# Kernel optimization log

Measured on AMD Instinct MI355X. Metric: run time of the kernel, lower is better.

## Reference

```python
import jax, jax.numpy as jnp
import numpy as np

K = 20
DEPTH = 4
EMB = 1024
NEG = 0.2   # LeakyReLU slope
EPS = 1e-5  # BatchNorm eps (inference mode: running_mean=0, running_var=1)


def _bn_lrelu(x, g, b):
    # inference BatchNorm over channel axis 1 with mean=0, var=1, then LeakyReLU(0.2)
    sh = [1] * x.ndim
    sh[1] = -1
    y = x * (g / jnp.sqrt(1.0 + EPS)).reshape(sh) + b.reshape(sh)
    return jnp.where(y >= 0, y, NEG * y)


def _attention_edge(x, Wq, Wk, Wv):
    # x: (G, N, C). Full self-attention, topk neighbor selection, EdgeConv features.
    C = x.shape[-1]
    q = x @ Wq.T
    k = x @ Wk.T
    v = x @ Wv.T
    att = jax.nn.softmax(jnp.einsum('gnc,gmc->gnm', q, k) / jnp.sqrt(jnp.float32(C)), axis=-1)
    out = jnp.einsum('gnm,gmc->gnc', att, v)
    idx = jax.lax.top_k(att, K)[1]                      # (G,N,K) neighbor indices
    xt = x + out                                        # residual: x + x_sa
    feat = jax.vmap(lambda a, i: a[i])(xt, idx)         # (G,N,K,C) gather
    ctr = jnp.broadcast_to(xt[:, :, None, :], feat.shape)
    return jnp.concatenate([feat - ctr, ctr], axis=-1)  # (G,N,K,2C)


def _seq_graph_feature(x, Wq, Wk, Wv):
    # x: (B, F, C, N) -> (B, 2C, F, N, K); vectorizes the per-sample Python loop
    B, F, C, N = x.shape
    xf = x.reshape(B * F, C, N).transpose(0, 2, 1)      # (G,N,C)
    e = _attention_edge(xf, Wq, Wk, Wv)                 # (G,N,K,2C)
    return e.reshape(B, F, N, K, 2 * C).transpose(0, 4, 1, 2, 3)


def setup_inputs() -> dict:
    key = jax.random.key(0)
    ks = jax.random.split(key, 16)
    d = {}
    d['x'] = jax.random.normal(ks[0], (8, 32, 3, 512), jnp.float32)
    d['Wq1'] = jax.random.normal(ks[1], (3, 3), jnp.float32) * 0.5
    d['Wk1'] = jax.random.normal(ks[2], (3, 3), jnp.float32) * 0.5
    d['Wv1'] = jax.random.normal(ks[3], (3, 3), jnp.float32) * 0.5
    d['Wq2'] = jax.random.normal(ks[4], (64, 64), jnp.float32) * 0.1
    d['Wk2'] = jax.random.normal(ks[5], (64, 64), jnp.float32) * 0.1
    d['Wv2'] = jax.random.normal(ks[6], (64, 64), jnp.float32) * 0.1
    d['conv1_w'] = jax.random.normal(ks[7], (64, 6, DEPTH, 3, 3), jnp.float32) * 0.1
    d['conv2_w'] = jax.random.normal(ks[8], (128, 128), jnp.float32) * 0.05
    d['conv5_w'] = jax.random.normal(ks[9], (EMB, 192), jnp.float32) * 0.05
    d['bn1_g'] = jax.random.uniform(ks[10], (64,), jnp.float32, 0.5, 1.5)
    d['bn1_b'] = jax.random.normal(ks[11], (64,), jnp.float32) * 0.1
    d['bn2_g'] = jax.random.uniform(ks[12], (128,), jnp.float32, 0.5, 1.5)
    d['bn2_b'] = jax.random.normal(ks[13], (128,), jnp.float32) * 0.1
    d['bn5_g'] = jax.random.uniform(ks[14], (EMB,), jnp.float32, 0.5, 1.5)
    d['bn5_b'] = jax.random.normal(ks[15], (EMB,), jnp.float32) * 0.1
    return d


def reference(x, Wq1, Wk1, Wv1, Wq2, Wk2, Wv2, conv1_w, conv2_w, conv5_w,
              bn1_g, bn1_b, bn2_g, bn2_b, bn5_g, bn5_b):
    y = _seq_graph_feature(x, Wq1, Wk1, Wv1)                      # (B,6,F,N,K)
    y = jax.lax.conv_general_dilated(
        y, conv1_w, window_strides=(DEPTH, 2, 1), padding='VALID',
        dimension_numbers=('NCDHW', 'OIDHW', 'NCDHW'))            # (B,64,F',N',K-2)
    y = _bn_lrelu(y, bn1_g, bn1_b)
    x1 = y.max(axis=-1)                                           # (B,64,F',N')
    x1p = x1.transpose(0, 2, 1, 3)                                # (B,F',64,N')
    y = _seq_graph_feature(x1p, Wq2, Wk2, Wv2)                    # (B,128,F',N',K)
    y = jnp.einsum('bcfnk,oc->bofnk', y, conv2_w)                 # 1x1x1 conv3d
    y = _bn_lrelu(y, bn2_g, bn2_b)
    x2 = y.max(axis=-1)                                           # (B,128,F',N')
    y = jnp.concatenate([x1, x2], axis=1)                         # (B,192,F',N')
    y = jnp.einsum('bcfn,oc->bofn', y, conv5_w)                   # 1x1 conv2d
    y = _bn_lrelu(y, bn5_g, bn5_b)
    emb = y.max(axis=-1).transpose(0, 2, 1)                       # (B,F',EMB)
    return emb
```

## Files before the change

### kernel.cpp

```cpp
#include <hip/hip_runtime.h>
#include <hip/hip_bf16.h>
#include <math.h>

typedef float f4 __attribute__((ext_vector_type(4)));

#define NEG 0.2f
#define BN_EPS 1e-5f

#define CE(K,A,B) { unsigned long long _x = K[A], _y = K[B]; bool _s = _x < _y; \
                    K[A] = _s ? _y : _x; K[B] = _s ? _x : _y; }

__device__ __forceinline__ float wred_max_f32(float v) {
  int x = __float_as_int(v), y;
#define STEPM(C) y = __builtin_amdgcn_update_dpp(x, x, C, 0xf, 0xf, false); \
  x = __float_as_int(fmaxf(__int_as_float(x), __int_as_float(y)));
  STEPM(0x111) STEPM(0x112) STEPM(0x114) STEPM(0x118) STEPM(0x142) STEPM(0x143)
#undef STEPM
  return __int_as_float(__builtin_amdgcn_readlane(x, 63));
}
__device__ __forceinline__ float wred_sum_f32(float v) {
  int x = __float_as_int(v), y;
#define STEPS(C) y = __builtin_amdgcn_update_dpp(0, x, C, 0xf, 0xf, true); \
  x = __float_as_int(__int_as_float(x) + __int_as_float(y));
  STEPS(0x111) STEPS(0x112) STEPS(0x114) STEPS(0x118) STEPS(0x142) STEPS(0x143)
#undef STEPS
  return __int_as_float(__builtin_amdgcn_readlane(x, 63));
}
__device__ __forceinline__ unsigned wred16_max_u32(unsigned v) {
  int x = (int)v, y;
#define STEPU(C) y = __builtin_amdgcn_update_dpp(x, x, C, 0xf, 0xf, false); \
  x = (int)((unsigned)x > (unsigned)y ? (unsigned)x : (unsigned)y);
  STEPU(0x111) STEPU(0x112) STEPU(0x114) STEPU(0x118)
#undef STEPU
  unsigned a0 = (unsigned)__builtin_amdgcn_readlane(x, 15);
  unsigned a1 = (unsigned)__builtin_amdgcn_readlane(x, 31);
  unsigned a2 = (unsigned)__builtin_amdgcn_readlane(x, 47);
  unsigned a3 = (unsigned)__builtin_amdgcn_readlane(x, 63);
  unsigned m01 = a0 > a1 ? a0 : a1;
  unsigned m23 = a2 > a3 ? a2 : a3;
  return m01 > m23 ? m01 : m23;
}

__device__ __forceinline__ unsigned sel_round8(unsigned (&hi)[8], unsigned (&lo)[8],
                                               bool do_pop) {
  unsigned gv = wred16_max_u32(hi[0]);
  unsigned long long tied = __ballot(hi[0] == gv);
  unsigned gl;
  if (__popcll(tied) == 1) {
    int wl = __ffsll((long long)tied) - 1;
    gl = (unsigned)__builtin_amdgcn_readlane((int)lo[0], wl);
  } else {
    gl = wred16_max_u32((hi[0] == gv) ? lo[0] : 0u);
  }
  if (do_pop) {
    bool win = (hi[0] == gv) && (lo[0] == gl);
    hi[0] = win ? hi[1] : hi[0]; lo[0] = win ? lo[1] : lo[0];
    hi[1] = win ? hi[2] : hi[1]; lo[1] = win ? lo[2] : lo[1];
    hi[2] = win ? hi[3] : hi[2]; lo[2] = win ? lo[3] : lo[2];
    hi[3] = win ? hi[4] : hi[3]; lo[3] = win ? lo[4] : lo[3];
    hi[4] = win ? hi[5] : hi[4]; lo[4] = win ? lo[5] : lo[4];
    hi[5] = win ? hi[6] : hi[5]; lo[5] = win ? lo[6] : lo[5];
    hi[6] = win ? hi[7] : hi[6]; lo[6] = win ? lo[7] : lo[6];
    hi[7] = win ? 0u    : hi[7]; lo[7] = win ? 0u    : lo[7];
  }
  return gl;
}
__device__ __forceinline__ unsigned sel_round4(unsigned (&hi)[4], unsigned (&lo)[4],
                                               bool do_pop) {
  unsigned gv = wred16_max_u32(hi[0]);
  unsigned long long tied = __ballot(hi[0] == gv);
  unsigned gl;
  if (__popcll(tied) == 1) {
    int wl = __ffsll((long long)tied) - 1;
    gl = (unsigned)__builtin_amdgcn_readlane((int)lo[0], wl);
  } else {
    gl = wred16_max_u32((hi[0] == gv) ? lo[0] : 0u);
  }
  if (do_pop) {
    bool win = (hi[0] == gv) && (lo[0] == gl);
    hi[0] = win ? hi[1] : hi[0]; lo[0] = win ? lo[1] : lo[0];
    hi[1] = win ? hi[2] : hi[1]; lo[1] = win ? lo[2] : lo[1];
    hi[2] = win ? hi[3] : hi[2]; lo[2] = win ? lo[3] : lo[2];
    hi[3] = win ? 0u    : hi[3]; lo[3] = win ? 0u    : lo[3];
  }
  return gl;
}

__global__ __launch_bounds__(256) void qkv1_k(const float* __restrict__ x,
    const float* __restrict__ Wk, const float* __restrict__ Wv,
    float* __restrict__ k1, float* __restrict__ v1) {
#pragma clang fp contract(off)
  int g = blockIdx.y;
  int n = blockIdx.x * 256 + threadIdx.x;
  const float* xr = x + (size_t)g * 1536;
  float x0 = xr[n], x1v = xr[512 + n], x2v = xr[1024 + n];
  f4 kd, vd;
#pragma unroll
  for (int o = 0; o < 3; ++o) {
    kd[o] = x0 * Wk[o*3+0] + x1v * Wk[o*3+1] + x2v * Wk[o*3+2];
    vd[o] = x0 * Wv[o*3+0] + x1v * Wv[o*3+1] + x2v * Wv[o*3+2];
  }
  kd[3] = 0.f; vd[3] = 0.f;
  *(f4*)(k1 + ((size_t)g * 512 + n) * 4) = kd;
  *(f4*)(v1 + ((size_t)g * 512 + n) * 4) = vd;
}

__global__ __launch_bounds__(256) void attn1_k(const float* __restrict__ x,
    const float* __restrict__ Wq, const float* __restrict__ k1,
    const float* __restrict__ v1, float* __restrict__ xt1p, int* __restrict__ idx1) {
  __shared__ f4 kl[512];
  __shared__ f4 vl[512];
  int t = threadIdx.x, g = blockIdx.y;
  int w = t >> 6, l = t & 63;
  int nb = blockIdx.x * 16;
  const f4* kgp = (const f4*)(k1 + (size_t)g * 2048);
  const f4* vgp = (const f4*)(v1 + (size_t)g * 2048);
  for (int i = t; i < 512; i += 256) { kl[i] = kgp[i]; vl[i] = vgp[i]; }
  __syncthreads();
  const float* xr = x + (size_t)g * 1536;
  for (int rp = 0; rp < 2; ++rp) {
    int nA = nb + rp * 8 + w;
    int nB = nA + 4;
    float xA0 = xr[nA], xA1 = xr[512 + nA], xA2 = xr[1024 + nA];
    float xB0 = xr[nB], xB1 = xr[512 + nB], xB2 = xr[1024 + nB];
    float qA0, qA1, qA2, qB0, qB1, qB2;
    float aA[8], aB[8];
    {
#pragma clang fp contract(off)
      qA0 = xA0*Wq[0] + xA1*Wq[1] + xA2*Wq[2];
      qA1 = xA0*Wq[3] + xA1*Wq[4] + xA2*Wq[5];
      qA2 = xA0*Wq[6] + xA1*Wq[7] + xA2*Wq[8];
      qB0 = xB0*Wq[0] + xB1*Wq[1] + xB2*Wq[2];
      qB1 = xB0*Wq[3] + xB1*Wq[4] + xB2*Wq[5];
      qB2 = xB0*Wq[6] + xB1*Wq[7] + xB2*Wq[8];
#pragma unroll
      for (int j = 0; j < 8; ++j) {
        f4 kk = kl[l + 64 * j];
        aA[j] = (qA0*kk[0] + qA1*kk[1] + qA2*kk[2]) / sqrtf(3.0f);
        aB[j] = (qB0*kk[0] + qB1*kk[1] + qB2*kk[2]) / sqrtf(3.0f);
      }
    }
    float mxA = aA[0], mxB = aB[0];
#pragma unroll
    for (int j = 1; j < 8; ++j) { mxA = fmaxf(mxA, aA[j]); mxB = fmaxf(mxB, aB[j]); }
    mxA = wred_max_f32(mxA); mxB = wred_max_f32(mxB);
    float wsA = 0.f, wsB = 0.f;
#pragma unroll
    for (int j = 0; j < 8; ++j) {
      aA[j] = expf(aA[j] - mxA); wsA += aA[j];
      aB[j] = expf(aB[j] - mxB); wsB += aB[j];
    }
    wsA = wred_sum_f32(wsA); wsB = wred_sum_f32(wsB);
#pragma unroll
    for (int j = 0; j < 8; ++j) { aA[j] = aA[j] / wsA; aB[j] = aB[j] / wsB; }
    float oA0 = 0.f, oA1 = 0.f, oA2 = 0.f, oB0 = 0.f, oB1 = 0.f, oB2 = 0.f;
#pragma unroll
    for (int j = 0; j < 8; ++j) {
      f4 vv = vl[l + 64 * j];
      oA0 += aA[j] * vv[0]; oA1 += aA[j] * vv[1]; oA2 += aA[j] * vv[2];
      oB0 += aB[j] * vv[0]; oB1 += aB[j] * vv[1]; oB2 += aB[j] * vv[2];
    }
    oA0 = wred_sum_f32(oA0); oA1 = wred_sum_f32(oA1); oA2 = wred_sum_f32(oA2);
    oB0 = wred_sum_f32(oB0); oB1 = wred_sum_f32(oB1); oB2 = wred_sum_f32(oB2);
    if (l == 0) {
      float* xo = xt1p + ((size_t)g * 512 + nA) * 4;
      xo[0] = xA0 + oA0; xo[1] = xA1 + oA1; xo[2] = xA2 + oA2;
      float* xo2 = xt1p + ((size_t)g * 512 + nB) * 4;
      xo2[0] = xB0 + oB0; xo2[1] = xB1 + oB1; xo2[2] = xB2 + oB2;
    }
    unsigned long long keyA[8], keyB[8];
#pragma unroll
    for (int j = 0; j < 8; ++j) {
      unsigned idx = (unsigned)(l + 64 * j);
      keyA[j] = ((unsigned long long)__float_as_uint(aA[j]) << 32) | (unsigned)(~idx);
      keyB[j] = ((unsigned long long)__float_as_uint(aB[j]) << 32) | (unsigned)(~idx);
    }
    CE(keyA,0,1) CE(keyA,2,3) CE(keyA,4,5) CE(keyA,6,7)
    CE(keyA,0,2) CE(keyA,1,3) CE(keyA,4,6) CE(keyA,5,7)
    CE(keyA,1,2) CE(keyA,5,6)
    CE(keyA,0,4) CE(keyA,1,5) CE(keyA,2,6) CE(keyA,3,7)
    CE(keyA,2,4) CE(keyA,3,5)
    CE(keyA,1,2) CE(keyA,3,4) CE(keyA,5,6)
    CE(keyB,0,1) CE(keyB,2,3) CE(keyB,4,5) CE(keyB,6,7)
    CE(keyB,0,2) CE(keyB,1,3) CE(keyB,4,6) CE(keyB,5,7)
    CE(keyB,1,2) CE(keyB,5,6)
    CE(keyB,0,4) CE(keyB,1,5) CE(keyB,2,6) CE(keyB,3,7)
    CE(keyB,2,4) CE(keyB,3,5)
    CE(keyB,1,2) CE(keyB,3,4) CE(keyB,5,6)
    unsigned hiA[8], loA[8], hiB[8], loB[8];
#pragma unroll
    for (int j = 0; j < 8; ++j) {
      hiA[j] = (unsigned)(keyA[j] >> 32); loA[j] = (unsigned)keyA[j];
      hiB[j] = (unsigned)(keyB[j] >> 32); loB[j] = (unsigned)keyB[j];
    }
    int* ioA = idx1 + ((size_t)g * 512 + nA) * 20;
    int* ioB = idx1 + ((size_t)g * 512 + nB) * 20;
    for (int kk = 0; kk < 20; ++kk) {
      unsigned gA = sel_round8(hiA, loA, kk < 19);
      unsigned gB = sel_round8(hiB, loB, kk < 19);
      if (l == 0) { ioA[kk] = (int)(~gA); ioB[kk] = (int)(~gB); }
    }
  }
}

__global__ __launch_bounds__(256) void conv1_k(const float* __restrict__ xt1p,
    const int* __restrict__ idx1, const float* __restrict__ w1,
    const float* __restrict__ bg, const float* __restrict__ bb,
    float* __restrict__ x1g) {
  __shared__ float wt[108][64];
  __shared__ float cwt[36][64];
  __shared__ __align__(16) float yfl[4][10][3][20];
  __shared__ float ycl[4][10][4];
  int t = threadIdx.x;
  int fp = blockIdx.y, b = blockIdx.z;
  int np0 = blockIdx.x * 16;
  int o = t & 63, part = t >> 6;
  for (int i = part; i < 108; i += 4) {
    int w3 = i % 3, rh = i / 3;
    int cc = rh / 12, dh = rh % 12;
    wt[i][o] = w1[o * 216 + cc * 36 + dh * 3 + w3];
  }
  for (int i = part; i < 36; i += 4) {
    int cc = i / 12, dh = i % 12;
    const float* ww = &w1[o * 216 + (cc + 3) * 36 + dh * 3];
    cwt[i][o] = ww[0] + ww[1] + ww[2];
  }
  int g2 = b * 8 + fp;
  for (int rnd = 0; rnd < 4; ++rnd) {
    int npr = np0 + rnd * 4;
    __syncthreads();
    for (int it = t; it < 800; it += 256) {
      int d = it / 200, rem = it % 200, nl = rem / 20, k = rem % 20;
      int n = 2 * npr + nl;
      if (n < 512) {
        int g = b * 32 + fp * 4 + d;
        int j = idx1[((size_t)g * 512 + n) * 20 + k];
        f4 vj = *(const f4*)(xt1p + ((size_t)g * 512 + j) * 4);
        f4 vc = *(const f4*)(xt1p + ((size_t)g * 512 + n) * 4);
        yfl[d][nl][0][k] = vj[0] - vc[0];
        yfl[d][nl][1][k] = vj[1] - vc[1];
        yfl[d][nl][2][k] = vj[2] - vc[2];
      } else {
        yfl[d][nl][0][k] = 0.f; yfl[d][nl][1][k] = 0.f; yfl[d][nl][2][k] = 0.f;
      }
    }
    if (t < 40) {
      int d = t / 10, nl = t % 10;
      int n = 2 * npr + nl;
      if (n < 512) {
        int g = b * 32 + fp * 4 + d;
        f4 vc = *(const f4*)(xt1p + ((size_t)g * 512 + n) * 4);
        ycl[d][nl][0] = vc[0]; ycl[d][nl][1] = vc[1]; ycl[d][nl][2] = vc[2];
      } else {
        ycl[d][nl][0] = 0.f; ycl[d][nl][1] = 0.f; ycl[d][nl][2] = 0.f;
      }
    }
    __syncthreads();
    int np = npr + part;
    if (np < 255) {
      float fa[18] = {0.f,0.f,0.f,0.f,0.f,0.f,0.f,0.f,0.f,
                      0.f,0.f,0.f,0.f,0.f,0.f,0.f,0.f,0.f};
      float ctr = 0.f;
      for (int cc = 0; cc < 3; ++cc) {
        for (int dh = 0; dh < 12; ++dh) {
          int d = dh / 3, h = dh % 3;
          int nl = 2 * part + h;
          int ib = (cc * 12 + dh) * 3;
          float w0 = wt[ib][o], w1v = wt[ib + 1][o], w2v = wt[ib + 2][o];
          ctr += ycl[d][nl][cc] * cwt[cc * 12 + dh][o];
          const f4* yr = (const f4*)&yfl[d][nl][cc][0];
          float y[20];
#pragma unroll
          for (int q = 0; q < 5; ++q) {
            f4 v = yr[q];
            y[4*q+0] = v[0]; y[4*q+1] = v[1]; y[4*q+2] = v[2]; y[4*q+3] = v[3];
          }
#pragma unroll
          for (int kp = 0; kp < 18; ++kp)
            fa[kp] += w0 * y[kp] + w1v * y[kp + 1] + w2v * y[kp + 2];
        }
      }
      float vmax = fa[0];
#pragma unroll
      for (int kp = 1; kp < 18; ++kp) vmax = fmaxf(vmax, fa[kp]);
      vmax += ctr;
      float sc = bg[o] / sqrtf(1.0f + BN_EPS);
      float z = sc * vmax + bb[o];
      if (z < 0.f) z *= NEG;
      x1g[((size_t)g2 * 255 + np) * 64 + o] = z;
    }
  }
}

__global__ __launch_bounds__(256) void qkv2_k(const float* __restrict__ x1g,
    const float* __restrict__ Wq, const float* __restrict__ Wk, const float* __restrict__ Wv,
    float* __restrict__ q2, float* __restrict__ k2, float* __restrict__ v2) {
  __shared__ float Wl[3][64 * 65];
  __shared__ float rowl[4][64];
  int t = threadIdx.x, g = blockIdx.y;
  int w = t >> 6, l = t & 63;
  for (int i = t; i < 4096; i += 256) {
    int r = i >> 6, c = i & 63;
    Wl[0][r * 65 + c] = Wq[i];
    Wl[1][r * 65 + c] = Wk[i];
    Wl[2][r * 65 + c] = Wv[i];
  }
  __syncthreads();
  for (int rr = 0; rr < 8; ++rr) {
    int n = blockIdx.x * 32 + rr * 4 + w;
    bool valid = n < 255;
    rowl[w][l] = valid ? x1g[((size_t)g * 255 + n) * 64 + l] : 0.f;
    float qa = 0.f, ka = 0.f, va = 0.f;
    for (int c = 0; c < 64; ++c) {
      float rv = rowl[w][c];
      qa += rv * Wl[0][l * 65 + c];
      ka += rv * Wl[1][l * 65 + c];
      va += rv * Wl[2][l * 65 + c];
    }
    if (valid) {
      size_t off = ((size_t)g * 255 + n) * 64 + l;
      q2[off] = qa; k2[off] = ka; v2[off] = va;
    }
  }
}

__global__ __launch_bounds__(256) void attn2_k(const float* __restrict__ q2,
    const float* __restrict__ k2, const float* __restrict__ v2,
    const float* __restrict__ x1g, float* __restrict__ xt2, int* __restrict__ idx2) {
  __shared__ __align__(16) float Kl[255 * 64];
  __shared__ __align__(16) float Vl[255 * 64];
  __shared__ __align__(16) float pl[4][4][256];
  __shared__ __align__(16) float ql[4][4][64];
  int t = threadIdx.x, g = blockIdx.y;
  int w = t >> 6, l = t & 63;
  int n0 = blockIdx.x * 64;
  const float* kg = k2 + (size_t)g * 16320;
  const float* vg = v2 + (size_t)g * 16320;
  for (int i = t; i < 4080; i += 256) {
    int m = i >> 4, c4 = (i & 15) << 2;
    f4 kv = *(const f4*)(kg + (size_t)i * 4);
    f4 vv = *(const f4*)(vg + (size_t)i * 4);
    *(f4*)&Kl[m * 64 + (c4 ^ ((m & 7) << 2))] = kv;
    *(f4*)&Vl[m * 64 + c4] = vv;
  }
  __syncthreads();
  for (int grp = 0; grp < 4; ++grp) {
    int rbase = n0 + w * 16 + grp * 4;
#pragma unroll
    for (int r = 0; r < 4; ++r) {
      int n = rbase + r;
      ql[w][r][l] = (n < 255) ? q2[((size_t)g * 255 + n) * 64 + l] : 0.f;
    }
    float s[4][4] = {};
    for (int c4 = 0; c4 < 64; c4 += 4) {
      f4 kv[4];
#pragma unroll
      for (int j = 0; j < 4; ++j) {
        int m = l + 64 * j;
        kv[j] = *(const f4*)&Kl[m * 64 + (c4 ^ ((m & 7) << 2))];
      }
#pragma unroll
      for (int r = 0; r < 4; ++r) {
        f4 qv = *(const f4*)&ql[w][r][c4];
#pragma unroll
        for (int j = 0; j < 4; ++j)
          s[r][j] += qv[0]*kv[j][0] + qv[1]*kv[j][1] + qv[2]*kv[j][2] + qv[3]*kv[j][3];
      }
    }
    unsigned Hi[4][4], Lo[4][4];
#pragma unroll
    for (int r = 0; r < 4; ++r) {
#pragma unroll
      for (int j = 0; j < 4; ++j) s[r][j] = s[r][j] / 8.0f;
      if (l == 63) s[r][3] = -1e30f;
      float mx = fmaxf(fmaxf(s[r][0], s[r][1]), fmaxf(s[r][2], s[r][3]));
      mx = wred_max_f32(mx);
      float ws = 0.f;
#pragma unroll
      for (int j = 0; j < 4; ++j) { s[r][j] = expf(s[r][j] - mx); ws += s[r][j]; }
      ws = wred_sum_f32(ws);
      unsigned long long key[4];
#pragma unroll
      for (int j = 0; j < 4; ++j) {
        s[r][j] = s[r][j] / ws;
        pl[w][r][64 * j + l] = s[r][j];
        key[j] = ((unsigned long long)__float_as_uint(s[r][j]) << 32)
               | (unsigned)(~(unsigned)(64 * j + l));
      }
      CE(key,0,1) CE(key,2,3) CE(key,0,2) CE(key,1,3) CE(key,1,2)
#pragma unroll
      for (int j = 0; j < 4; ++j) {
        Hi[r][j] = (unsigned)(key[j] >> 32); Lo[r][j] = (unsigned)key[j];
      }
    }
    float acc[4] = {0.f, 0.f, 0.f, 0.f};
    for (int m4 = 0; m4 < 256; m4 += 4) {
      f4 pv[4];
#pragma unroll
      for (int r = 0; r < 4; ++r) pv[r] = *(const f4*)&pl[w][r][m4];
      float v0 = Vl[(m4 + 0) * 64 + l];
      float v1 = Vl[(m4 + 1) * 64 + l];
      float v2v = Vl[(m4 + 2) * 64 + l];
      float v3 = Vl[(m4 + 3) * 64 + l];
#pragma unroll
      for (int r = 0; r < 4; ++r)
        acc[r] += pv[r][0]*v0 + pv[r][1]*v1 + pv[r][2]*v2v + pv[r][3]*v3;
    }
#pragma unroll
    for (int r = 0; r < 4; ++r) {
      int n = rbase + r;
      if (n < 255) {
        size_t off = ((size_t)g * 255 + n) * 64 + l;
        xt2[off] = x1g[off] + acc[r];
      }
    }
    int* io0 = idx2 + ((size_t)g * 255 + rbase + 0) * 20;
    int* io1 = idx2 + ((size_t)g * 255 + rbase + 1) * 20;
    int* io2 = idx2 + ((size_t)g * 255 + rbase + 2) * 20;
    int* io3 = idx2 + ((size_t)g * 255 + rbase + 3) * 20;
    for (int kk = 0; kk < 20; ++kk) {
      unsigned g0 = sel_round4(Hi[0], Lo[0], kk < 19);
      unsigned g1 = sel_round4(Hi[1], Lo[1], kk < 19);
      unsigned g2v = sel_round4(Hi[2], Lo[2], kk < 19);
      unsigned g3 = sel_round4(Hi[3], Lo[3], kk < 19);
      if (l == 0) {
        if (rbase + 0 < 255) io0[kk] = (int)(~g0);
        if (rbase + 1 < 255) io1[kk] = (int)(~g1);
        if (rbase + 2 < 255) io2[kk] = (int)(~g2v);
        if (rbase + 3 < 255) io3[kk] = (int)(~g3);
      }
    }
  }
}

__global__ __launch_bounds__(256) void conv2_k(const float* __restrict__ xt2,
    const int* __restrict__ idx2, const float* __restrict__ w2,
    const float* __restrict__ bg, const float* __restrict__ bb,
    float* __restrict__ x2g) {
  __shared__ __align__(16) float w2h[64 * 128];
  __shared__ float rows[8][21][64];
  int t = threadIdx.x, g = blockIdx.y;
  int n0 = blockIdx.x * 8;
  for (int i = t; i < 10752; i += 256) {
    int pos = i / 1344, rem = i % 1344, r = rem >> 6, c = rem & 63;
    int n = n0 + pos;
    float v = 0.f;
    if (n < 255) {
      if (r < 20) {
        int j = idx2[((size_t)g * 255 + n) * 20 + r];
        v = xt2[((size_t)g * 255 + j) * 64 + c];
      } else v = xt2[((size_t)g * 255 + n) * 64 + c];
    }
    rows[pos][r][c] = v;
  }
  for (int i = t; i < 8192; i += 256) {
    int o2 = i >> 6, c = i & 63;
    w2h[c * 128 + (o2 ^ (c & 28))] = w2[o2 * 128 + c];
  }
  __syncthreads();
  int os = t & 31, np = t >> 5;
  float acc[4][20] = {};
  float t1[4] = {0.f, 0.f, 0.f, 0.f};
  for (int c = 0; c < 64; ++c) {
    f4 wq = *(const f4*)&w2h[c * 128 + ((os * 4) ^ (c & 28))];
    float cv = rows[np][20][c];
#pragma unroll
    for (int i = 0; i < 4; ++i) t1[i] += wq[i] * cv;
#pragma unroll
    for (int j = 0; j < 20; ++j) {
      float rv = rows[np][j][c];
#pragma unroll
      for (int i = 0; i < 4; ++i) acc[i][j] += wq[i] * rv;
    }
  }
  __syncthreads();
  for (int i = t; i < 8192; i += 256) {
    int o2 = i >> 6, c = i & 63;
    w2h[c * 128 + (o2 ^ (c & 28))] = w2[o2 * 128 + 64 + c];
  }
  __syncthreads();
  float t2[4] = {0.f, 0.f, 0.f, 0.f};
  for (int c = 0; c < 64; ++c) {
    f4 wq = *(const f4*)&w2h[c * 128 + ((os * 4) ^ (c & 28))];
    float cv = rows[np][20][c];
#pragma unroll
    for (int i = 0; i < 4; ++i) t2[i] += wq[i] * cv;
  }
  int n = n0 + np;
  f4 res;
#pragma unroll
  for (int i = 0; i < 4; ++i) {
    float vm = -1e30f;
#pragma unroll
    for (int j = 0; j < 20; ++j) vm = fmaxf(vm, acc[i][j]);
    vm += t2[i] - t1[i];
    int o = os * 4 + i;
    float sc = bg[o] / sqrtf(1.0f + BN_EPS);
    float z = sc * vm + bb[o];
    if (z < 0.f) z *= NEG;
    res[i] = z;
  }
  if (n < 255)
    *(f4*)&x2g[((size_t)g * 255 + n) * 128 + os * 4] = res;
}

__global__ __launch_bounds__(256) void conv5_k(const float* __restrict__ x1g,
    const float* __restrict__ x2g, const float* __restrict__ w5,
    const float* __restrict__ bg, const float* __restrict__ bb,
    float* __restrict__ out) {
  __shared__ __align__(16) float w5h[96 * 64];
  __shared__ float colh[32][97];
  __shared__ float red[16][64];
  int t = threadIdx.x;
  int ot = blockIdx.x, fp = blockIdx.y, b = blockIdx.z;
  size_t rowbase = ((size_t)b * 8 + fp) * 255;
  int os = t & 15, ns = t >> 4;
  float vm[4] = {-1e30f, -1e30f, -1e30f, -1e30f};
  for (int gh = 0; gh < 2; ++gh) {
    float acc[4][4][2] = {};
    for (int ch = 0; ch < 2; ++ch) {
      __syncthreads();
      for (int i = t; i < 6144; i += 256) {
        int oL = i / 96, c = i % 96;
        w5h[c * 64 + (oL ^ (c & 28))] = w5[((size_t)(ot * 64 + oL)) * 192 + ch * 96 + c];
      }
#pragma unroll
      for (int gl = 0; gl < 4; ++gl) {
        int grp = gh * 4 + gl;
        __syncthreads();
        for (int i = t; i < 3072; i += 256) {
          int nl = i / 96, c = i % 96;
          int n = grp * 32 + nl;
          float v = 0.f;
          if (n < 255) {
            int cc = ch * 96 + c;
            v = (cc < 64) ? x1g[(rowbase + n) * 64 + cc]
                          : x2g[(rowbase + n) * 128 + (cc - 64)];
          }
          colh[nl][c] = v;
        }
        __syncthreads();
        for (int c = 0; c < 96; ++c) {
          f4 wq = *(const f4*)&w5h[c * 64 + ((os * 4) ^ (c & 28))];
#pragma unroll
          for (int vv = 0; vv < 2; ++vv) {
            float cvv = colh[ns * 2 + vv][c];
#pragma unroll
            for (int u = 0; u < 4; ++u) acc[gl][u][vv] += wq[u] * cvv;
          }
        }
      }
    }
#pragma unroll
    for (int gl = 0; gl < 4; ++gl)
#pragma unroll
      for (int vv = 0; vv < 2; ++vv) {
        int n = (gh * 4 + gl) * 32 + ns * 2 + vv;
        if (n < 255)
#pragma unroll
          for (int u = 0; u < 4; ++u) vm[u] = fmaxf(vm[u], acc[gl][u][vv]);
      }
  }
#pragma unroll
  for (int u = 0; u < 4; ++u) red[ns][os * 4 + u] = vm[u];
  __syncthreads();
  if (t < 64) {
    float m = -1e30f;
#pragma unroll
    for (int q = 0; q < 16; ++q) m = fmaxf(m, red[q][t]);
    int o = ot * 64 + t;
    float sc = bg[o] / sqrtf(1.0f + BN_EPS);
    float z = sc * m + bb[o];
    if (z < 0.f) z *= NEG;
    out[((size_t)b * 8 + fp) * 1024 + o] = z;
  }
}

extern "C" void kernel_launch(void* const* d_in, const int* in_sizes, int n_in,
                              void* d_out, int out_size, void* d_ws, size_t ws_size,
                              hipStream_t stream) {
  const float* x   = (const float*)d_in[0];
  const float* Wq1 = (const float*)d_in[1];
  const float* Wk1 = (const float*)d_in[2];
  const float* Wv1 = (const float*)d_in[3];
  const float* Wq2 = (const float*)d_in[4];
  const float* Wk2 = (const float*)d_in[5];
  const float* Wv2 = (const float*)d_in[6];
  const float* w1  = (const float*)d_in[7];
  const float* w2  = (const float*)d_in[8];
  const float* w5  = (const float*)d_in[9];
  const float* bg1 = (const float*)d_in[10];
  const float* bb1 = (const float*)d_in[11];
  const float* bg2 = (const float*)d_in[12];
  const float* bb2 = (const float*)d_in[13];
  const float* bg5 = (const float*)d_in[14];
  const float* bb5 = (const float*)d_in[15];
  float* out = (float*)d_out;
  float* ws  = (float*)d_ws;

  float* k1   = ws;
  float* v1   = ws + 524288;
  float* x1g  = ws;
  float* xt1p = ws + 1048576;
  int*   idx1 = (int*)(ws + 1572864);
  float* q2   = ws + 4194304;
  float* k2   = ws + 5238784;
  float* v2   = ws + 6283264;
  float* xt2  = ws + 7327744;
  int*   idx2 = (int*)(ws + 8372224);
  float* x2g  = ws + 8698624;

  qkv1_k<<<dim3(2, 256), 256, 0, stream>>>(x, Wk1, Wv1, k1, v1);
  attn1_k<<<dim3(32, 256), 256, 0, stream>>>(x, Wq1, k1, v1, xt1p, idx1);
  conv1_k<<<dim3(16, 8, 8), 256, 0, stream>>>(xt1p, idx1, w1, bg1, bb1, x1g);
  qkv2_k<<<dim3(8, 64), 256, 0, stream>>>(x1g, Wq2, Wk2, Wv2, q2, k2, v2);
  attn2_k<<<dim3(4, 64), 256, 0, stream>>>(q2, k2, v2, x1g, xt2, idx2);
  conv2_k<<<dim3(32, 64), 256, 0, stream>>>(xt2, idx2, w2, bg2, bb2, x2g);
  conv5_k<<<dim3(16, 8, 8), 256, 0, stream>>>(x1g, x2g, w5, bg5, bb5, out);
}
```

Baseline: 876.5 us.

## Fuse K/V projection into attn1 and process four rows per wave

```diff
diff --git a/kernel.cpp b/kernel.cpp
--- a/kernel.cpp
+++ b/kernel.cpp
@@ -86,119 +86,130 @@
   return gl;
 }
 
-__global__ __launch_bounds__(256) void qkv1_k(const float* __restrict__ x,
-    const float* __restrict__ Wk, const float* __restrict__ Wv,
-    float* __restrict__ k1, float* __restrict__ v1) {
-#pragma clang fp contract(off)
-  int g = blockIdx.y;
-  int n = blockIdx.x * 256 + threadIdx.x;
-  const float* xr = x + (size_t)g * 1536;
-  float x0 = xr[n], x1v = xr[512 + n], x2v = xr[1024 + n];
-  f4 kd, vd;
-#pragma unroll
-  for (int o = 0; o < 3; ++o) {
-    kd[o] = x0 * Wk[o*3+0] + x1v * Wk[o*3+1] + x2v * Wk[o*3+2];
-    vd[o] = x0 * Wv[o*3+0] + x1v * Wv[o*3+1] + x2v * Wv[o*3+2];
-  }
-  kd[3] = 0.f; vd[3] = 0.f;
-  *(f4*)(k1 + ((size_t)g * 512 + n) * 4) = kd;
-  *(f4*)(v1 + ((size_t)g * 512 + n) * 4) = vd;
-}
-
-__global__ __launch_bounds__(256) void attn1_k(const float* __restrict__ x,
-    const float* __restrict__ Wq, const float* __restrict__ k1,
-    const float* __restrict__ v1, float* __restrict__ xt1p, int* __restrict__ idx1) {
+__global__ __launch_bounds__(256, 4) void attn1_k(const float* __restrict__ x,
+    const float* __restrict__ Wq, const float* __restrict__ Wk,
+    const float* __restrict__ Wv, float* __restrict__ xt1p, int* __restrict__ idx1) {
   __shared__ f4 kl[512];
   __shared__ f4 vl[512];
   int t = threadIdx.x, g = blockIdx.y;
   int w = t >> 6, l = t & 63;
   int nb = blockIdx.x * 16;
-  const f4* kgp = (const f4*)(k1 + (size_t)g * 2048);
-  const f4* vgp = (const f4*)(v1 + (size_t)g * 2048);
-  for (int i = t; i < 512; i += 256) { kl[i] = kgp[i]; vl[i] = vgp[i]; }
+  const float* xr = x + (size_t)g * 1536;
+  {
+#pragma clang fp contract(off)
+    for (int i = t; i < 512; i += 256) {
+      float x0 = xr[i], x1v = xr[512 + i], x2v = xr[1024 + i];
+      f4 kd, vd;
+#pragma unroll
+      for (int o = 0; o < 3; ++o) {
+        kd[o] = x0 * Wk[o*3+0] + x1v * Wk[o*3+1] + x2v * Wk[o*3+2];
+        vd[o] = x0 * Wv[o*3+0] + x1v * Wv[o*3+1] + x2v * Wv[o*3+2];
+      }
+      kd[3] = 0.f; vd[3] = 0.f;
+      kl[i] = kd; vl[i] = vd;
+    }
+  }
   __syncthreads();
-  const float* xr = x + (size_t)g * 1536;
-  for (int rp = 0; rp < 2; ++rp) {
-    int nA = nb + rp * 8 + w;
-    int nB = nA + 4;
-    float xA0 = xr[nA], xA1 = xr[512 + nA], xA2 = xr[1024 + nA];
-    float xB0 = xr[nB], xB1 = xr[512 + nB], xB2 = xr[1024 + nB];
-    float qA0, qA1, qA2, qB0, qB1, qB2;
-    float aA[8], aB[8];
-    {
+  int n0 = nb + w * 4;
+  float a[4][8];
+  float xv[4][3];
+  {
 #pragma clang fp contract(off)
-      qA0 = xA0*Wq[0] + xA1*Wq[1] + xA2*Wq[2];
-      qA1 = xA0*Wq[3] + xA1*Wq[4] + xA2*Wq[5];
-      qA2 = xA0*Wq[6] + xA1*Wq[7] + xA2*Wq[8];
-      qB0 = xB0*Wq[0] + xB1*Wq[1] + xB2*Wq[2];
-      qB1 = xB0*Wq[3] + xB1*Wq[4] + xB2*Wq[5];
-      qB2 = xB0*Wq[6] + xB1*Wq[7] + xB2*Wq[8];
-#pragma unroll
-      for (int j = 0; j < 8; ++j) {
-        f4 kk = kl[l + 64 * j];
-        aA[j] = (qA0*kk[0] + qA1*kk[1] + qA2*kk[2]) / sqrtf(3.0f);
-        aB[j] = (qB0*kk[0] + qB1*kk[1] + qB2*kk[2]) / sqrtf(3.0f);
-      }
-    }
-    float mxA = aA[0], mxB = aB[0];
-#pragma unroll
-    for (int j = 1; j < 8; ++j) { mxA = fmaxf(mxA, aA[j]); mxB = fmaxf(mxB, aB[j]); }
-    mxA = wred_max_f32(mxA); mxB = wred_max_f32(mxB);
-    float wsA = 0.f, wsB = 0.f;
+    float q[4][3];
+#pragma unroll
+    for (int r = 0; r < 4; ++r) {
+      int n = n0 + r;
+      xv[r][0] = xr[n]; xv[r][1] = xr[512 + n]; xv[r][2] = xr[1024 + n];
+      q[r][0] = xv[r][0]*Wq[0] + xv[r][1]*Wq[1] + xv[r][2]*Wq[2];
+      q[r][1] = xv[r][0]*Wq[3] + xv[r][1]*Wq[4] + xv[r][2]*Wq[5];
+      q[r][2] = xv[r][0]*Wq[6] + xv[r][1]*Wq[7] + xv[r][2]*Wq[8];
+    }
 #pragma unroll
     for (int j = 0; j < 8; ++j) {
-      aA[j] = expf(aA[j] - mxA); wsA += aA[j];
-      aB[j] = expf(aB[j] - mxB); wsB += aB[j];
-    }
-    wsA = wred_sum_f32(wsA); wsB = wred_sum_f32(wsB);
-#pragma unroll
-    for (int j = 0; j < 8; ++j) { aA[j] = aA[j] / wsA; aB[j] = aB[j] / wsB; }
-    float oA0 = 0.f, oA1 = 0.f, oA2 = 0.f, oB0 = 0.f, oB1 = 0.f, oB2 = 0.f;
+      f4 kk = kl[l + 64 * j];
+#pragma unroll
+      for (int r = 0; r < 4; ++r)
+        a[r][j] = (q[r][0]*kk[0] + q[r][1]*kk[1] + q[r][2]*kk[2]) / sqrtf(3.0f);
+    }
+  }
+  float mx[4];
+#pragma unroll
+  for (int r = 0; r < 4; ++r) {
+    float m = a[r][0];
+#pragma unroll
+    for (int j = 1; j < 8; ++j) m = fmaxf(m, a[r][j]);
+    mx[r] = m;
+  }
+#pragma unroll
+  for (int r = 0; r < 4; ++r) mx[r] = wred_max_f32(mx[r]);
+  float ws[4] = {0.f, 0.f, 0.f, 0.f};
+#pragma unroll
+  for (int r = 0; r < 4; ++r)
+#pragma unroll
+    for (int j = 0; j < 8; ++j) { a[r][j] = expf(a[r][j] - mx[r]); ws[r] += a[r][j]; }
+#pragma unroll
+  for (int r = 0; r < 4; ++r) ws[r] = wred_sum_f32(ws[r]);
+#pragma unroll
+  for (int r = 0; r < 4; ++r)
+#pragma unroll
+    for (int j = 0; j < 8; ++j) a[r][j] = a[r][j] / ws[r];
+  float ov[4][3] = {};
+#pragma unroll
+  for (int j = 0; j < 8; ++j) {
+    f4 vv = vl[l + 64 * j];
+#pragma unroll
+    for (int r = 0; r < 4; ++r) {
+      ov[r][0] += a[r][j] * vv[0];
+      ov[r][1] += a[r][j] * vv[1];
+      ov[r][2] += a[r][j] * vv[2];
+    }
+  }
+#pragma unroll
+  for (int r = 0; r < 4; ++r) {
+    ov[r][0] = wred_sum_f32(ov[r][0]);
+    ov[r][1] = wred_sum_f32(ov[r][1]);
+    ov[r][2] = wred_sum_f32(ov[r][2]);
+  }
+  if (l == 0) {
+#pragma unroll
+    for (int r = 0; r < 4; ++r) {
+      float* xo = xt1p + ((size_t)g * 512 + n0 + r) * 4;
+      xo[0] = xv[r][0] + ov[r][0];
+      xo[1] = xv[r][1] + ov[r][1];
+      xo[2] = xv[r][2] + ov[r][2];
+    }
+  }
+  unsigned hi[4][8], lo[4][8];
+#pragma unroll
+  for (int r = 0; r < 4; ++r) {
+    unsigned long long key[8];
+#pragma unroll
+    for (int j = 0; j < 8; ++j)
+      key[j] = ((unsigned long long)__float_as_uint(a[r][j]) << 32)
+             | (unsigned)(~(unsigned)(l + 64 * j));
+    CE(key,0,1) CE(key,2,3) CE(key,4,5) CE(key,6,7)
+    CE(key,0,2) CE(key,1,3) CE(key,4,6) CE(key,5,7)
+    CE(key,1,2) CE(key,5,6)
+    CE(key,0,4) CE(key,1,5) CE(key,2,6) CE(key,3,7)
+    CE(key,2,4) CE(key,3,5)
+    CE(key,1,2) CE(key,3,4) CE(key,5,6)
 #pragma unroll
     for (int j = 0; j < 8; ++j) {
-      f4 vv = vl[l + 64 * j];
-      oA0 += aA[j] * vv[0]; oA1 += aA[j] * vv[1]; oA2 += aA[j] * vv[2];
-      oB0 += aB[j] * vv[0]; oB1 += aB[j] * vv[1]; oB2 += aB[j] * vv[2];
-    }
-    oA0 = wred_sum_f32(oA0); oA1 = wred_sum_f32(oA1); oA2 = wred_sum_f32(oA2);
-    oB0 = wred_sum_f32(oB0); oB1 = wred_sum_f32(oB1); oB2 = wred_sum_f32(oB2);
+      hi[r][j] = (unsigned)(key[j] >> 32); lo[r][j] = (unsigned)key[j];
+    }
+  }
+  int* io0 = idx1 + ((size_t)g * 512 + n0 + 0) * 20;
+  int* io1 = idx1 + ((size_t)g * 512 + n0 + 1) * 20;
+  int* io2 = idx1 + ((size_t)g * 512 + n0 + 2) * 20;
+  int* io3 = idx1 + ((size_t)g * 512 + n0 + 3) * 20;
+  for (int kk = 0; kk < 20; ++kk) {
+    unsigned g0 = sel_round8(hi[0], lo[0], kk < 19);
+    unsigned g1 = sel_round8(hi[1], lo[1], kk < 19);
+    unsigned g2 = sel_round8(hi[2], lo[2], kk < 19);
+    unsigned g3 = sel_round8(hi[3], lo[3], kk < 19);
     if (l == 0) {
-      float* xo = xt1p + ((size_t)g * 512 + nA) * 4;
-      xo[0] = xA0 + oA0; xo[1] = xA1 + oA1; xo[2] = xA2 + oA2;
-      float* xo2 = xt1p + ((size_t)g * 512 + nB) * 4;
-      xo2[0] = xB0 + oB0; xo2[1] = xB1 + oB1; xo2[2] = xB2 + oB2;
-    }
-    unsigned long long keyA[8], keyB[8];
-#pragma unroll
-    for (int j = 0; j < 8; ++j) {
-      unsigned idx = (unsigned)(l + 64 * j);
-      keyA[j] = ((unsigned long long)__float_as_uint(aA[j]) << 32) | (unsigned)(~idx);
-      keyB[j] = ((unsigned long long)__float_as_uint(aB[j]) << 32) | (unsigned)(~idx);
-    }
-    CE(keyA,0,1) CE(keyA,2,3) CE(keyA,4,5) CE(keyA,6,7)
-    CE(keyA,0,2) CE(keyA,1,3) CE(keyA,4,6) CE(keyA,5,7)
-    CE(keyA,1,2) CE(keyA,5,6)
-    CE(keyA,0,4) CE(keyA,1,5) CE(keyA,2,6) CE(keyA,3,7)
-    CE(keyA,2,4) CE(keyA,3,5)
-    CE(keyA,1,2) CE(keyA,3,4) CE(keyA,5,6)
-    CE(keyB,0,1) CE(keyB,2,3) CE(keyB,4,5) CE(keyB,6,7)
-    CE(keyB,0,2) CE(keyB,1,3) CE(keyB,4,6) CE(keyB,5,7)
-    CE(keyB,1,2) CE(keyB,5,6)
-    CE(keyB,0,4) CE(keyB,1,5) CE(keyB,2,6) CE(keyB,3,7)
-    CE(keyB,2,4) CE(keyB,3,5)
-    CE(keyB,1,2) CE(keyB,3,4) CE(keyB,5,6)
-    unsigned hiA[8], loA[8], hiB[8], loB[8];
-#pragma unroll
-    for (int j = 0; j < 8; ++j) {
-      hiA[j] = (unsigned)(keyA[j] >> 32); loA[j] = (unsigned)keyA[j];
-      hiB[j] = (unsigned)(keyB[j] >> 32); loB[j] = (unsigned)keyB[j];
-    }
-    int* ioA = idx1 + ((size_t)g * 512 + nA) * 20;
-    int* ioB = idx1 + ((size_t)g * 512 + nB) * 20;
-    for (int kk = 0; kk < 20; ++kk) {
-      unsigned gA = sel_round8(hiA, loA, kk < 19);
-      unsigned gB = sel_round8(hiB, loB, kk < 19);
-      if (l == 0) { ioA[kk] = (int)(~gA); ioB[kk] = (int)(~gB); }
+      io0[kk] = (int)(~g0); io1[kk] = (int)(~g1);
+      io2[kk] = (int)(~g2); io3[kk] = (int)(~g3);
     }
   }
 }
@@ -598,8 +609,6 @@
   float* out = (float*)d_out;
   float* ws  = (float*)d_ws;
 
-  float* k1   = ws;
-  float* v1   = ws + 524288;
   float* x1g  = ws;
   float* xt1p = ws + 1048576;
   int*   idx1 = (int*)(ws + 1572864);
@@ -610,8 +619,7 @@
   int*   idx2 = (int*)(ws + 8372224);
   float* x2g  = ws + 8698624;
 
-  qkv1_k<<<dim3(2, 256), 256, 0, stream>>>(x, Wk1, Wv1, k1, v1);
-  attn1_k<<<dim3(32, 256), 256, 0, stream>>>(x, Wq1, k1, v1, xt1p, idx1);
+  attn1_k<<<dim3(32, 256), 256, 0, stream>>>(x, Wq1, Wk1, Wv1, xt1p, idx1);
   conv1_k<<<dim3(16, 8, 8), 256, 0, stream>>>(xt1p, idx1, w1, bg1, bb1, x1g);
   qkv2_k<<<dim3(8, 64), 256, 0, stream>>>(x1g, Wq2, Wk2, Wv2, q2, k2, v2);
   attn2_k<<<dim3(4, 64), 256, 0, stream>>>(q2, k2, v2, x1g, xt2, idx2);
```

Result: slower. 897.4 us (+2.4%).
